# Kernel tuning notes

Measured on AMD Instinct MI355X. Metric: run time of the kernel, lower is better.

Reference implementation:

```python
import jax, jax.numpy as jnp
import numpy as np

B, S, H = 2, 2048, 4096
NH, NKV, HD = 32, 8, 128
THETA = 1000000.0
NEG = jnp.finfo(jnp.float32).min


def setup_inputs() -> dict:
    key = jax.random.key(0)
    ks = jax.random.split(key, 9)
    s = 0.02
    return {
        "hidden_states": jax.random.normal(ks[0], (B, S, H), jnp.float32),
        "position_ids": jnp.tile(jnp.arange(S, dtype=jnp.int32)[None, :], (B, 1)),
        "Wq": jax.random.normal(ks[1], (NH * HD, H), jnp.float32) * s,
        "bq": jax.random.normal(ks[2], (NH * HD,), jnp.float32) * s,
        "Wk": jax.random.normal(ks[3], (NKV * HD, H), jnp.float32) * s,
        "bk": jax.random.normal(ks[4], (NKV * HD,), jnp.float32) * s,
        "Wv": jax.random.normal(ks[5], (NKV * HD, H), jnp.float32) * s,
        "bv": jax.random.normal(ks[6], (NKV * HD,), jnp.float32) * s,
        "Wo": jax.random.normal(ks[7], (H, H), jnp.float32) * s,
        "bo": jax.random.normal(ks[8], (H,), jnp.float32) * s,
    }


def _rotate_half_interleaved(x):
    # y[..., ::2] = -x[..., 1::2]; y[..., 1::2] = x[..., ::2]
    x2 = x.reshape(*x.shape[:-1], -1, 2)
    y = jnp.stack([-x2[..., 1], x2[..., 0]], axis=-1)
    return y.reshape(x.shape)


def reference(hidden_states, position_ids, Wq, bq, Wk, bk, Wv, bv, Wo, bo):
    bsz, q_len, _ = hidden_states.shape
    q = (hidden_states @ Wq.T + bq).reshape(bsz, q_len, NH, HD).transpose(0, 2, 1, 3)
    k = (hidden_states @ Wk.T + bk).reshape(bsz, q_len, NKV, HD).transpose(0, 2, 1, 3)
    v = (hidden_states @ Wv.T + bv).reshape(bsz, q_len, NKV, HD).transpose(0, 2, 1, 3)

    # rotary embedding (interleaved / repeat_interleave variant)
    inv_freq = 1.0 / (THETA ** (jnp.arange(0, HD, 2, dtype=jnp.float32) / HD))
    freqs = position_ids.astype(jnp.float32)[:, :, None] * inv_freq[None, None, :]  # [B,S,HD/2]
    emb = jnp.repeat(freqs, 2, axis=-1)  # [B,S,HD]
    cos = jnp.cos(emb)[:, None, :, :]  # [B,1,S,HD]
    sin = jnp.sin(emb)[:, None, :, :]
    q = q * cos + _rotate_half_interleaved(q) * sin
    k = k * cos + _rotate_half_interleaved(k) * sin

    # GQA: repeat KV heads (repeat_interleave on head axis)
    n_rep = NH // NKV
    k = jnp.repeat(k, n_rep, axis=1)
    v = jnp.repeat(v, n_rep, axis=1)

    scores = jnp.einsum("bhqd,bhkd->bhqk", q, k) / np.sqrt(HD).astype(np.float32)
    causal = jnp.tril(jnp.ones((q_len, q_len), dtype=bool))
    scores = jnp.where(causal[None, None, :, :], scores, NEG)
    attn = jax.nn.softmax(scores.astype(jnp.float32), axis=-1).astype(q.dtype)
    out = jnp.einsum("bhqk,bhkd->bhqd", attn, v)
    out = out.transpose(0, 2, 1, 3).reshape(bsz, q_len, H)
    return out @ Wo.T + bo
```

## Files before the change

### kernel.cpp

```cpp
#include <hip/hip_runtime.h>
#include <stdint.h>

typedef __bf16 bf16x8 __attribute__((ext_vector_type(8)));
typedef float f32x4 __attribute__((ext_vector_type(4)));
typedef float f32x16 __attribute__((ext_vector_type(16)));

#define S_LEN 2048
#define NKVH 8
#define HDIM 128
#define MROWS 4096
#define LDQKV 6144
#define SCALE 0.08838834764831845f
#define C_LOG2 0.1275405707067851f
#define THR_RAW 62.7f

__device__ __forceinline__ unsigned short f2bf(float f) {
  unsigned u = __float_as_uint(f);
  u += 0x7FFFu + ((u >> 16) & 1u);
  return (unsigned short)(u >> 16);
}
__device__ __forceinline__ float bf2f(unsigned short h) {
  return __uint_as_float(((unsigned)h) << 16);
}

__device__ __forceinline__ void gload16(const unsigned short* g, unsigned short* l) {
  __builtin_amdgcn_global_load_lds(
      (__attribute__((address_space(1))) void*)(g),
      (__attribute__((address_space(3))) void*)(l), 16, 0, 0);
}

__global__ void cast_f32_bf16(const float4* __restrict__ in, ushort4* __restrict__ out, int n4) {
  int i = blockIdx.x * 256 + threadIdx.x;
  const int stride = gridDim.x * 256;
  for (; i < n4; i += stride) {
    float4 v = in[i];
    ushort4 o;
    o.x = f2bf(v.x); o.y = f2bf(v.y); o.z = f2bf(v.z); o.w = f2bf(v.w);
    out[i] = o;
  }
}

template <int OUTF>
__global__ __launch_bounds__(512, 2)
void gemm256(const unsigned short* __restrict__ A,
             const unsigned short* __restrict__ Bw,
             const float* __restrict__ bias,
             void* __restrict__ C,
             int M, int N, int K) {
  __shared__ unsigned short lds[2][4][8192];

  const int t = threadIdx.x;
  const int lane = t & 63;
  const int w = t >> 6;
  const int wr = w >> 2, wc = w & 3;
  const int row16 = lane & 15, kgrp = lane >> 4;
  const int m0 = blockIdx.y * 256, n0 = blockIdx.x * 256;

  const int riu = t >> 3;
  const int col = (((t & 7) ^ (riu & 7)) << 3);
  const int rB0 = (riu & 31) + ((riu >> 5) << 6);
  const unsigned short* pA = A + (size_t)(m0 + riu) * K + col;
  const unsigned short* pB = Bw + (size_t)(n0 + rB0) * K + col;

#define STG(nb_, u_, src_)                                                  \
  {                                                                         \
    gload16((src_), &lds[nb_][u_][t * 8]);                                  \
    gload16((src_) + (size_t)128 * K, &lds[nb_][u_][4096 + t * 8]);         \
  }

  const int sw = row16 & 7;
  const int abase = (wr * 64 + row16) * 64;
  const int bbase = (wc * 32 + row16) * 64;

  f32x4 acc[8][4];
#pragma unroll
  for (int i = 0; i < 8; i++)
#pragma unroll
    for (int j = 0; j < 4; j++) acc[i][j] = (f32x4){0.f, 0.f, 0.f, 0.f};

  bf16x8 afr[4][2], bfr[2][2][2];
  const int NT = K >> 6;

  STG(0, 0, pA);
  STG(0, 1, pB);
  STG(0, 2, pB + (size_t)32 * K);
  STG(0, 3, pA + (size_t)64 * K);

  for (int T = 0; T < NT; ++T) {
    const int cb = T & 1, nb = cb ^ 1;
    const unsigned short* Lc = &lds[cb][0][0];
    const size_t kk = (size_t)(T + 1) << 6;
    const bool st = (T + 1 < NT);

    asm volatile("s_waitcnt vmcnt(4)\n\ts_barrier" ::: "memory");
    if (st) STG(nb, 0, pA + kk);
#pragma unroll
    for (int mi = 0; mi < 4; mi++)
#pragma unroll
      for (int ks = 0; ks < 2; ks++)
        afr[mi][ks] = *(const bf16x8*)(Lc + abase + mi * 1024 + ((((ks << 2) + kgrp) ^ sw) << 3));
#pragma unroll
    for (int nj = 0; nj < 2; nj++)
#pragma unroll
      for (int ks = 0; ks < 2; ks++)
        bfr[0][nj][ks] = *(const bf16x8*)(Lc + 8192 + bbase + nj * 1024 + ((((ks << 2) + kgrp) ^ sw) << 3));
    __builtin_amdgcn_s_setprio(1);
#pragma unroll
    for (int mi = 0; mi < 4; mi++)
#pragma unroll
      for (int nj = 0; nj < 2; nj++)
#pragma unroll
        for (int ks = 0; ks < 2; ks++)
          acc[mi][nj] = __builtin_amdgcn_mfma_f32_16x16x32_bf16(afr[mi][ks], bfr[0][nj][ks], acc[mi][nj], 0, 0, 0);
    __builtin_amdgcn_s_setprio(0);

    if (st) {
      asm volatile("s_waitcnt vmcnt(4)\n\ts_barrier" ::: "memory");
      STG(nb, 1, pB + kk);
    } else {
      asm volatile("s_waitcnt vmcnt(2)\n\ts_barrier" ::: "memory");
    }
#pragma unroll
    for (int nj = 0; nj < 2; nj++)
#pragma unroll
      for (int ks = 0; ks < 2; ks++)
        bfr[1][nj][ks] = *(const bf16x8*)(Lc + 16384 + bbase + nj * 1024 + ((((ks << 2) + kgrp) ^ sw) << 3));
    __builtin_amdgcn_s_setprio(1);
#pragma unroll
    for (int mi = 0; mi < 4; mi++)
#pragma unroll
      for (int nj = 0; nj < 2; nj++)
#pragma unroll
        for (int ks = 0; ks < 2; ks++)
          acc[mi][2 + nj] = __builtin_amdgcn_mfma_f32_16x16x32_bf16(afr[mi][ks], bfr[1][nj][ks], acc[mi][2 + nj], 0, 0, 0);
    __builtin_amdgcn_s_setprio(0);

    if (st) {
      asm volatile("s_waitcnt vmcnt(4)\n\ts_barrier" ::: "memory");
      STG(nb, 2, pB + (size_t)32 * K + kk);
    } else {
      asm volatile("s_waitcnt vmcnt(0)\n\ts_barrier" ::: "memory");
    }
#pragma unroll
    for (int mi = 0; mi < 4; mi++)
#pragma unroll
      for (int ks = 0; ks < 2; ks++)
        afr[mi][ks] = *(const bf16x8*)(Lc + 24576 + abase + mi * 1024 + ((((ks << 2) + kgrp) ^ sw) << 3));
    __builtin_amdgcn_s_setprio(1);
#pragma unroll
    for (int mi = 0; mi < 4; mi++)
#pragma unroll
      for (int nj = 0; nj < 2; nj++)
#pragma unroll
        for (int ks = 0; ks < 2; ks++)
          acc[4 + mi][2 + nj] = __builtin_amdgcn_mfma_f32_16x16x32_bf16(afr[mi][ks], bfr[1][nj][ks], acc[4 + mi][2 + nj], 0, 0, 0);
    __builtin_amdgcn_s_setprio(0);

    if (st) {
      asm volatile("s_waitcnt vmcnt(4)\n\ts_barrier" ::: "memory");
      STG(nb, 3, pA + (size_t)64 * K + kk);
    } else {
      asm volatile("s_barrier" ::: "memory");
    }
    __builtin_amdgcn_s_setprio(1);
#pragma unroll
    for (int mi = 0; mi < 4; mi++)
#pragma unroll
      for (int nj = 0; nj < 2; nj++)
#pragma unroll
        for (int ks = 0; ks < 2; ks++)
          acc[4 + mi][nj] = __builtin_amdgcn_mfma_f32_16x16x32_bf16(afr[mi][ks], bfr[0][nj][ks], acc[4 + mi][nj], 0, 0, 0);
    __builtin_amdgcn_s_setprio(0);
  }
#undef STG

#pragma unroll
  for (int MI = 0; MI < 8; MI++) {
#pragma unroll
    for (int NJ = 0; NJ < 4; NJ++) {
      const int gr = m0 + wr * 128 + MI * 16 + kgrp * 4;
      const int gc = n0 + wc * 64 + NJ * 16 + row16;
      const float bv = bias[gc];
#pragma unroll
      for (int jj = 0; jj < 4; jj++) {
        float v = acc[MI][NJ][jj] + bv;
        if (OUTF) ((float*)C)[(size_t)(gr + jj) * N + gc] = v;
        else ((unsigned short*)C)[(size_t)(gr + jj) * N + gc] = f2bf(v);
      }
    }
  }
}

__global__ void rope_kernel(unsigned short* __restrict__ X,
                            const int* __restrict__ pos_ids,
                            int ncols, int ld) {
  const int perrow = ncols >> 3;
  int idx = blockIdx.x * 256 + threadIdx.x;
  const int row = idx / perrow;
  const int c0 = (idx - row * perrow) << 3;
  const float pos = (float)pos_ids[row];
  unsigned short* p = X + (size_t)row * ld + c0;
  uint4 v = *(uint4*)p;
  unsigned short* e = (unsigned short*)&v;
  const int p0 = (c0 & 127) >> 1;
#pragma unroll
  for (int q = 0; q < 4; ++q) {
    const float inv = exp2f(-(float)(p0 + q) * (19.931568569324174f / 64.f));
    const float fr = pos * inv;
    float sn, cs;
    __sincosf(fr, &sn, &cs);
    const float xe = bf2f(e[2 * q]);
    const float xo = bf2f(e[2 * q + 1]);
    e[2 * q]     = f2bf(xe * cs - xo * sn);
    e[2 * q + 1] = f2bf(xo * cs + xe * sn);
  }
  *(uint4*)p = v;
}

__global__ void transpose_v(const unsigned short* __restrict__ V, int ldv,
                            unsigned short* __restrict__ Vt) {
  __shared__ unsigned short tile[32][40];
  const int t = threadIdx.x;
  const int n0 = blockIdx.x * 32;
  const int m0 = blockIdx.y * 32;
  const int r = t >> 3;
  const int c = (t & 7) << 2;
  const unsigned short* src = V + (size_t)(m0 + r) * ldv + n0 + c;
  ushort4 d = *(const ushort4*)src;
  tile[r][c] = d.x; tile[r][c + 1] = d.y; tile[r][c + 2] = d.z; tile[r][c + 3] = d.w;
  __syncthreads();
  const int b = m0 >> 11;
  unsigned short* dst = Vt + (size_t)(b * 1024 + n0 + r) * 2048 + (m0 & 2047) + c;
  ushort4 o;
  o.x = tile[c][r]; o.y = tile[c + 1][r]; o.z = tile[c + 2][r]; o.w = tile[c + 3][r];
  *(ushort4*)dst = o;
}

__global__ __launch_bounds__(512, 2)
void attn_kernel2(const unsigned short* __restrict__ QKV,
                  const unsigned short* __restrict__ Vt,
                  unsigned short* __restrict__ O) {
  __shared__ unsigned short sK[2][64 * 128];
  __shared__ unsigned short sV[2][128 * 64];

  const int t = threadIdx.x;
  const int lane = t & 63;
  const int w = t >> 6;
  const int l31 = lane & 31;
  const int hi = lane >> 5;
  const int qt = 7 - blockIdx.x;
  const int bh = blockIdx.y;
  const int b = bh >> 5, h = bh & 31;
  const int kh = h >> 2;
  const int q0 = qt * 256;
  const int qw = q0 + w * 32;
  const int qg = qw + l31;

  const int ntiles = (q0 + 256) >> 6;
  const int myTiles = (qw + 95) >> 6;

  const int krow0 = t >> 4;
  const int kslot = t & 15;
  const int vrow0 = t >> 3;
  const int vslot = t & 7;
  const unsigned short* Kp = QKV + (size_t)(b * S_LEN) * LDQKV + 4096 + kh * HDIM;
  const unsigned short* Vp = Vt + (size_t)(b * 1024 + kh * HDIM) * 2048;
  const int ksw = (kslot ^ (krow0 & 7)) << 3;
  const int vsw = (vslot ^ (vrow0 & 7)) << 3;
  const unsigned short* KpA = Kp + (size_t)krow0 * LDQKV + ksw;
  const unsigned short* KpB = Kp + (size_t)(krow0 + 32) * LDQKV + ksw;
  const unsigned short* VpA = Vp + (size_t)vrow0 * 2048 + vsw;
  const unsigned short* VpB = Vp + (size_t)(vrow0 + 64) * 2048 + vsw;

#define STAGE(bufi, kv0m)                                              \
  {                                                                    \
    gload16(KpA + (size_t)(kv0m)*LDQKV, &sK[bufi][t * 8]);             \
    gload16(KpB + (size_t)(kv0m)*LDQKV, &sK[bufi][4096 + t * 8]);      \
    gload16(VpA + (kv0m), &sV[bufi][t * 8]);                           \
    gload16(VpB + (kv0m), &sV[bufi][4096 + t * 8]);                    \
  }

  bf16x8 qf[8];
  {
    const unsigned short* qb = QKV + (size_t)(b * S_LEN + qw + l31) * LDQKV + h * HDIM + hi * 8;
#pragma unroll
    for (int kd = 0; kd < 8; kd++) qf[kd] = *(const bf16x8*)(qb + kd * 16);
  }

  f32x16 o[4];
#pragma unroll
  for (int nt = 0; nt < 4; nt++)
#pragma unroll
    for (int r = 0; r < 16; r++) o[nt][r] = 0.f;
  float m = -1e30f, lsum = 0.f;

  const int rw7 = (l31 & 7) << 4;
  const int kswz = (hi << 4) ^ rw7;
  const int kbase0 = l31 * 128;
  const int vbase = l31 * 64;

  STAGE(0, 0);
  int buf = 0;
  for (int it = 0; it < ntiles; ++it) {
    if (it + 1 < ntiles) {
      STAGE(buf ^ 1, (it + 1) << 6);
      asm volatile("s_waitcnt vmcnt(4)" ::: "memory");
    } else {
      asm volatile("s_waitcnt vmcnt(0)" ::: "memory");
    }
    __builtin_amdgcn_s_barrier();

    if (it < myTiles) {
      const unsigned short* sKc = &sK[buf][0];
      const unsigned short* sVc = &sV[buf][0];
      const int kv0 = it << 6;

      f32x16 st[2];
#pragma unroll
      for (int r = 0; r < 16; r++) { st[0][r] = 0.f; st[1][r] = 0.f; }
      __builtin_amdgcn_s_setprio(1);
#pragma unroll
      for (int kd = 0; kd < 8; kd++) {
        bf16x8 k0 = *(const bf16x8*)(sKc + kbase0 + (((kd << 5) ^ kswz) >> 1));
        bf16x8 k1 = *(const bf16x8*)(sKc + 4096 + kbase0 + (((kd << 5) ^ kswz) >> 1));
        st[0] = __builtin_amdgcn_mfma_f32_32x32x16_bf16(k0, qf[kd], st[0], 0, 0, 0);
        st[1] = __builtin_amdgcn_mfma_f32_32x32x16_bf16(k1, qf[kd], st[1], 0, 0, 0);
      }
      __builtin_amdgcn_s_setprio(0);

      if (it == myTiles - 1) {
#pragma unroll
        for (int s2 = 0; s2 < 2; s2++)
#pragma unroll
          for (int r = 0; r < 16; r++) {
            const int kvg = kv0 + s2 * 32 + (r & 3) + 8 * (r >> 2) + 4 * hi;
            if (kvg > qg) st[s2][r] = -1e30f;
          }
      }

      float tmax = st[0][0];
#pragma unroll
      for (int r = 1; r < 16; r++) tmax = fmaxf(tmax, st[0][r]);
#pragma unroll
      for (int r = 0; r < 16; r++) tmax = fmaxf(tmax, st[1][r]);
      tmax = fmaxf(tmax, __shfl_xor(tmax, 32));

      if (!__all(tmax <= m + THR_RAW)) {
        const float mnew = fmaxf(m, tmax);
        const float corr = exp2f((m - mnew) * C_LOG2);
        lsum *= corr;
#pragma unroll
        for (int r = 0; r < 16; r++) {
          const int src = (r & 3) + 8 * (r >> 2) + 4 * hi;
          const float cr = __shfl(corr, src);
#pragma unroll
          for (int nt = 0; nt < 4; nt++) o[nt][r] *= cr;
        }
        m = mnew;
      }
      const float mC = m * C_LOG2;

#pragma unroll
      for (int s2 = 0; s2 < 2; s2++)
#pragma unroll
        for (int r = 0; r < 16; r++) st[s2][r] = exp2f(fmaf(st[s2][r], C_LOG2, -mC));
      float tsum = st[0][0];
#pragma unroll
      for (int r = 1; r < 16; r++) tsum += st[0][r];
#pragma unroll
      for (int r = 0; r < 16; r++) tsum += st[1][r];
      tsum += __shfl_xor(tsum, 32);
      lsum += tsum;

      bf16x8 pa[4];
#pragma unroll
      for (int s2 = 0; s2 < 2; s2++) {
        unsigned pw[8];
#pragma unroll
        for (int i = 0; i < 8; i++)
          asm("v_cvt_pk_bf16_f32 %0, %1, %2" : "=v"(pw[i]) : "v"(st[s2][2 * i]), "v"(st[s2][2 * i + 1]));
        const unsigned x0 = (unsigned)__shfl_xor((int)pw[0], 32);
        const unsigned x1 = (unsigned)__shfl_xor((int)pw[1], 32);
        const unsigned x2 = (unsigned)__shfl_xor((int)pw[2], 32);
        const unsigned x3 = (unsigned)__shfl_xor((int)pw[3], 32);
        const unsigned x4 = (unsigned)__shfl_xor((int)pw[4], 32);
        const unsigned x5 = (unsigned)__shfl_xor((int)pw[5], 32);
        const unsigned x6 = (unsigned)__shfl_xor((int)pw[6], 32);
        const unsigned x7 = (unsigned)__shfl_xor((int)pw[7], 32);
        union { unsigned u[4]; bf16x8 v; } u0, u1;
        u0.u[0] = hi ? x2 : pw[0];
        u0.u[1] = hi ? x3 : pw[1];
        u0.u[2] = hi ? pw[2] : x0;
        u0.u[3] = hi ? pw[3] : x1;
        u1.u[0] = hi ? x6 : pw[4];
        u1.u[1] = hi ? x7 : pw[5];
        u1.u[2] = hi ? pw[6] : x4;
        u1.u[3] = hi ? pw[7] : x5;
        pa[2 * s2] = u0.v; pa[2 * s2 + 1] = u1.v;
      }

      __builtin_amdgcn_s_setprio(1);
#pragma unroll
      for (int nt = 0; nt < 4; nt++) {
        const unsigned short* vr = sVc + vbase + nt * 2048;
#pragma unroll
        for (int ks = 0; ks < 4; ks++) {
          bf16x8 vb = *(const bf16x8*)(vr + (((ks << 5) ^ kswz) >> 1));
          o[nt] = __builtin_amdgcn_mfma_f32_32x32x16_bf16(pa[ks], vb, o[nt], 0, 0, 0);
        }
      }
      __builtin_amdgcn_s_setprio(0);
    }

    asm volatile("" ::: "memory");
    __builtin_amdgcn_s_barrier();
    buf ^= 1;
  }

  const float linv = 1.0f / lsum;
#pragma unroll
  for (int r = 0; r < 16; r++) {
    const int qr = (r & 3) + 8 * (r >> 2) + 4 * hi;
    const float lr = __shfl(linv, qr);
    unsigned short* orow = O + (size_t)(b * S_LEN + qw + qr) * 4096 + h * HDIM + l31;
#pragma unroll
    for (int nt = 0; nt < 4; nt++) orow[nt * 32] = f2bf(o[nt][r] * lr);
  }
#undef STAGE
}

extern "C" void kernel_launch(void* const* d_in, const int* in_sizes, int n_in,
                              void* d_out, int out_size, void* d_ws, size_t ws_size,
                              hipStream_t stream) {
  const float* hs = (const float*)d_in[0];
  const int*  pos = (const int*)d_in[1];
  const float* Wq = (const float*)d_in[2];
  const float* bq = (const float*)d_in[3];
  const float* Wk = (const float*)d_in[4];
  const float* bk = (const float*)d_in[5];
  const float* Wv = (const float*)d_in[6];
  const float* bv = (const float*)d_in[7];
  const float* Wo = (const float*)d_in[8];
  const float* bo = (const float*)d_in[9];
  float* out = (float*)d_out;

  char* ws = (char*)d_ws;
  unsigned short* hbf  = (unsigned short*)(ws);
  unsigned short* Wbuf = (unsigned short*)(ws + 33554432);
  unsigned short* QKV  = (unsigned short*)(ws + 83886080);
  unsigned short* Vtb  = (unsigned short*)(ws + 134217728);
  float*          biasb= (float*)(ws + 142606336);

  cast_f32_bf16<<<2048, 256, 0, stream>>>((const float4*)hs, (ushort4*)hbf, 4194304);
  cast_f32_bf16<<<2048, 256, 0, stream>>>((const float4*)Wq, (ushort4*)Wbuf, 4194304);
  cast_f32_bf16<<<1024, 256, 0, stream>>>((const float4*)Wk, (ushort4*)(Wbuf + 16777216), 1048576);
  cast_f32_bf16<<<1024, 256, 0, stream>>>((const float4*)Wv, (ushort4*)(Wbuf + 20971520), 1048576);
  hipMemcpyAsync(biasb, bq, 4096 * 4, hipMemcpyDeviceToDevice, stream);
  hipMemcpyAsync(biasb + 4096, bk, 1024 * 4, hipMemcpyDeviceToDevice, stream);
  hipMemcpyAsync(biasb + 5120, bv, 1024 * 4, hipMemcpyDeviceToDevice, stream);

  gemm256<0><<<dim3(24, 16), 512, 0, stream>>>(hbf, Wbuf, biasb, QKV, MROWS, LDQKV, 4096);

  cast_f32_bf16<<<2048, 256, 0, stream>>>((const float4*)Wo, (ushort4*)Wbuf, 4194304);

  rope_kernel<<<8192, 256, 0, stream>>>(QKV, pos, 4096, LDQKV);
  rope_kernel<<<2048, 256, 0, stream>>>(QKV + 4096, pos, 1024, LDQKV);

  transpose_v<<<dim3(32, 128), 256, 0, stream>>>(QKV + 5120, LDQKV, Vtb);

  attn_kernel2<<<dim3(8, 64), 512, 0, stream>>>(QKV, Vtb, hbf);

  gemm256<1><<<dim3(16, 16), 512, 0, stream>>>(hbf, Wbuf, bo, out, MROWS, 4096, 4096);
}
```

Measured before the change: 613.9 us.

## Replace double-buffered GEMM LDS staging with a 10-slot ring buffer prefetching deeper

The GEMM's two-buffer, four-unit LDS staging is replaced by a 10-slot circular buffer. Prefetch now runs up to two K-tiles ahead, with waits loosened to vmcnt(8), so more global loads are in flight and MFMA stalls on memory should shrink. LDS use grows from 128KB to 160KB per block, which may limit occupancy under launch_bounds(512,2). The slot rotation and wait counts are delicate and could cause races.

Result: no change. 624.8 us (+1.8%).

```diff
diff --git a/kernel.cpp b/kernel.cpp
--- a/kernel.cpp
+++ b/kernel.cpp
@@ -47,7 +47,7 @@
              const float* __restrict__ bias,
              void* __restrict__ C,
              int M, int N, int K) {
-  __shared__ unsigned short lds[2][4][8192];
+  __shared__ unsigned short lds[10 * 8192];
 
   const int t = threadIdx.x;
   const int lane = t & 63;
@@ -62,10 +62,10 @@
   const unsigned short* pA = A + (size_t)(m0 + riu) * K + col;
   const unsigned short* pB = Bw + (size_t)(n0 + rB0) * K + col;
 
-#define STG(nb_, u_, src_)                                                  \
+#define STGS(sl_, src_)                                                     \
   {                                                                         \
-    gload16((src_), &lds[nb_][u_][t * 8]);                                  \
-    gload16((src_) + (size_t)128 * K, &lds[nb_][u_][4096 + t * 8]);         \
+    gload16((src_), &lds[(sl_) * 8192 + t * 8]);                            \
+    gload16((src_) + (size_t)128 * K, &lds[(sl_) * 8192 + 4096 + t * 8]);   \
   }
 
   const int sw = row16 & 7;
@@ -81,29 +81,44 @@
   bf16x8 afr[4][2], bfr[2][2][2];
   const int NT = K >> 6;
 
-  STG(0, 0, pA);
-  STG(0, 1, pB);
-  STG(0, 2, pB + (size_t)32 * K);
-  STG(0, 3, pA + (size_t)64 * K);
-
+  STGS(0, pA);
+  STGS(1, pB);
+  STGS(2, pB + (size_t)32 * K);
+  STGS(3, pA + (size_t)64 * K);
+  STGS(4, pA + 64);
+  STGS(5, pB + 64);
+
+  int rb = 0;
   for (int T = 0; T < NT; ++T) {
-    const int cb = T & 1, nb = cb ^ 1;
-    const unsigned short* Lc = &lds[cb][0][0];
-    const size_t kk = (size_t)(T + 1) << 6;
-    const bool st = (T + 1 < NT);
-
-    asm volatile("s_waitcnt vmcnt(4)\n\ts_barrier" ::: "memory");
-    if (st) STG(nb, 0, pA + kk);
+    int s1 = rb + 1; if (s1 >= 10) s1 -= 10;
+    int s2 = rb + 2; if (s2 >= 10) s2 -= 10;
+    int s3 = rb + 3; if (s3 >= 10) s3 -= 10;
+    int s6 = rb + 6; if (s6 >= 10) s6 -= 10;
+    int s7 = rb + 7; if (s7 >= 10) s7 -= 10;
+    int s8 = rb + 8; if (s8 >= 10) s8 -= 10;
+    int s9 = rb + 9; if (s9 >= 10) s9 -= 10;
+    const bool st1 = (T < NT - 1);
+    const bool st2 = (T < NT - 2);
+    const size_t k1 = (size_t)(T + 1) << 6;
+    const size_t k2 = (size_t)(T + 2) << 6;
+    const unsigned short* U0 = &lds[rb * 8192];
+    const unsigned short* U1 = &lds[s1 * 8192];
+    const unsigned short* U2 = &lds[s2 * 8192];
+    const unsigned short* U3 = &lds[s3 * 8192];
+
+    if (st1) { asm volatile("s_waitcnt vmcnt(8)\n\ts_barrier" ::: "memory"); }
+    else     { asm volatile("s_waitcnt vmcnt(4)\n\ts_barrier" ::: "memory"); }
+    if (st1) STGS(s6, pB + (size_t)32 * K + k1);
 #pragma unroll
     for (int mi = 0; mi < 4; mi++)
 #pragma unroll
       for (int ks = 0; ks < 2; ks++)
-        afr[mi][ks] = *(const bf16x8*)(Lc + abase + mi * 1024 + ((((ks << 2) + kgrp) ^ sw) << 3));
+        afr[mi][ks] = *(const bf16x8*)(U0 + abase + mi * 1024 + ((((ks << 2) + kgrp) ^ sw) << 3));
 #pragma unroll
     for (int nj = 0; nj < 2; nj++)
 #pragma unroll
       for (int ks = 0; ks < 2; ks++)
-        bfr[0][nj][ks] = *(const bf16x8*)(Lc + 8192 + bbase + nj * 1024 + ((((ks << 2) + kgrp) ^ sw) << 3));
+        bfr[0][nj][ks] = *(const bf16x8*)(U1 + bbase + nj * 1024 + ((((ks << 2) + kgrp) ^ sw) << 3));
     __builtin_amdgcn_s_setprio(1);
 #pragma unroll
     for (int mi = 0; mi < 4; mi++)
@@ -114,17 +129,14 @@
           acc[mi][nj] = __builtin_amdgcn_mfma_f32_16x16x32_bf16(afr[mi][ks], bfr[0][nj][ks], acc[mi][nj], 0, 0, 0);
     __builtin_amdgcn_s_setprio(0);
 
-    if (st) {
-      asm volatile("s_waitcnt vmcnt(4)\n\ts_barrier" ::: "memory");
-      STG(nb, 1, pB + kk);
-    } else {
-      asm volatile("s_waitcnt vmcnt(2)\n\ts_barrier" ::: "memory");
-    }
+    if (st1) { asm volatile("s_waitcnt vmcnt(8)\n\ts_barrier" ::: "memory"); }
+    else     { asm volatile("s_waitcnt vmcnt(2)\n\ts_barrier" ::: "memory"); }
+    if (st1) STGS(s7, pA + (size_t)64 * K + k1);
 #pragma unroll
     for (int nj = 0; nj < 2; nj++)
 #pragma unroll
       for (int ks = 0; ks < 2; ks++)
-        bfr[1][nj][ks] = *(const bf16x8*)(Lc + 16384 + bbase + nj * 1024 + ((((ks << 2) + kgrp) ^ sw) << 3));
+        bfr[1][nj][ks] = *(const bf16x8*)(U2 + bbase + nj * 1024 + ((((ks << 2) + kgrp) ^ sw) << 3));
     __builtin_amdgcn_s_setprio(1);
 #pragma unroll
     for (int mi = 0; mi < 4; mi++)
@@ -135,17 +147,14 @@
           acc[mi][2 + nj] = __builtin_amdgcn_mfma_f32_16x16x32_bf16(afr[mi][ks], bfr[1][nj][ks], acc[mi][2 + nj], 0, 0, 0);
     __builtin_amdgcn_s_setprio(0);
 
-    if (st) {
-      asm volatile("s_waitcnt vmcnt(4)\n\ts_barrier" ::: "memory");
-      STG(nb, 2, pB + (size_t)32 * K + kk);
-    } else {
-      asm volatile("s_waitcnt vmcnt(0)\n\ts_barrier" ::: "memory");
-    }
+    if (st1) { asm volatile("s_waitcnt vmcnt(8)\n\ts_barrier" ::: "memory"); }
+    else     { asm volatile("s_waitcnt vmcnt(0)\n\ts_barrier" ::: "memory"); }
+    if (st2) STGS(s8, pA + k2);
 #pragma unroll
     for (int mi = 0; mi < 4; mi++)
 #pragma unroll
       for (int ks = 0; ks < 2; ks++)
-        afr[mi][ks] = *(const bf16x8*)(Lc + 24576 + abase + mi * 1024 + ((((ks << 2) + kgrp) ^ sw) << 3));
+        afr[mi][ks] = *(const bf16x8*)(U3 + abase + mi * 1024 + ((((ks << 2) + kgrp) ^ sw) << 3));
     __builtin_amdgcn_s_setprio(1);
 #pragma unroll
     for (int mi = 0; mi < 4; mi++)
@@ -156,12 +165,7 @@
           acc[4 + mi][2 + nj] = __builtin_amdgcn_mfma_f32_16x16x32_bf16(afr[mi][ks], bfr[1][nj][ks], acc[4 + mi][2 + nj], 0, 0, 0);
     __builtin_amdgcn_s_setprio(0);
 
-    if (st) {
-      asm volatile("s_waitcnt vmcnt(4)\n\ts_barrier" ::: "memory");
-      STG(nb, 3, pA + (size_t)64 * K + kk);
-    } else {
-      asm volatile("s_barrier" ::: "memory");
-    }
+    if (st2) STGS(s9, pB + k2);
     __builtin_amdgcn_s_setprio(1);
 #pragma unroll
     for (int mi = 0; mi < 4; mi++)
@@ -171,8 +175,10 @@
         for (int ks = 0; ks < 2; ks++)
           acc[4 + mi][nj] = __builtin_amdgcn_mfma_f32_16x16x32_bf16(afr[mi][ks], bfr[0][nj][ks], acc[4 + mi][nj], 0, 0, 0);
     __builtin_amdgcn_s_setprio(0);
-  }
-#undef STG
+
+    rb += 4; if (rb >= 10) rb -= 10;
+  }
+#undef STGS
 
 #pragma unroll
   for (int MI = 0; MI < 8; MI++) {
```

## Split QKV projection into Q GEMM and separate 128-row-tile KV GEMM

Applied to the files above, without the earlier changes.

The fused QKV GEMM previously ran 24x16=384 tiles of 256x256, which is a poor fit for the GPU's compute-unit count (1.5 waves). Now Q uses 256 tiles of 256x256, and K/V use a new gemm128 kernel with 128x256 tiles (256 blocks) and triple-buffered LDS. This aims to fix the wave-quantization tail. The cost is an extra launch, a second kernel design to maintain, and lower arithmetic intensity per tile in the KV part.

Result: faster. 587.0 us (-4.4%).

```diff
diff --git a/kernel.cpp b/kernel.cpp
--- a/kernel.cpp
+++ b/kernel.cpp
@@ -46,7 +46,7 @@
              const unsigned short* __restrict__ Bw,
              const float* __restrict__ bias,
              void* __restrict__ C,
-             int M, int N, int K) {
+             int ldc, int K) {
   __shared__ unsigned short lds[2][4][8192];
 
   const int t = threadIdx.x;
@@ -184,8 +184,106 @@
 #pragma unroll
       for (int jj = 0; jj < 4; jj++) {
         float v = acc[MI][NJ][jj] + bv;
-        if (OUTF) ((float*)C)[(size_t)(gr + jj) * N + gc] = v;
-        else ((unsigned short*)C)[(size_t)(gr + jj) * N + gc] = f2bf(v);
+        if (OUTF) ((float*)C)[(size_t)(gr + jj) * ldc + gc] = v;
+        else ((unsigned short*)C)[(size_t)(gr + jj) * ldc + gc] = f2bf(v);
+      }
+    }
+  }
+}
+
+template <int OUTF>
+__global__ __launch_bounds__(512, 2)
+void gemm128(const unsigned short* __restrict__ A,
+             const unsigned short* __restrict__ Bw,
+             const float* __restrict__ bias,
+             void* __restrict__ C,
+             int ldc, int K) {
+  __shared__ unsigned short lds[3 * 24576];
+
+  const int t = threadIdx.x;
+  const int lane = t & 63;
+  const int w = t >> 6;
+  const int wr = w >> 2, wc = w & 3;
+  const int row16 = lane & 15, kgrp = lane >> 4;
+  const int m0 = blockIdx.y * 128, n0 = blockIdx.x * 256;
+
+  const int riu = t >> 3;
+  const int col = (((t & 7) ^ (riu & 7)) << 3);
+  const unsigned short* pA = A + (size_t)(m0 + riu) * K + col;
+  const unsigned short* pB = Bw + (size_t)(n0 + riu) * K + col;
+
+#define STG6(bo_, kk_)                                                      \
+  {                                                                         \
+    gload16(pA + (kk_), &lds[(bo_) + t * 8]);                               \
+    gload16(pA + (size_t)64 * K + (kk_), &lds[(bo_) + 4096 + t * 8]);       \
+    gload16(pB + (kk_), &lds[(bo_) + 8192 + t * 8]);                        \
+    gload16(pB + (size_t)64 * K + (kk_), &lds[(bo_) + 12288 + t * 8]);      \
+    gload16(pB + (size_t)128 * K + (kk_), &lds[(bo_) + 16384 + t * 8]);     \
+    gload16(pB + (size_t)192 * K + (kk_), &lds[(bo_) + 20480 + t * 8]);     \
+  }
+
+  const int sw = row16 & 7;
+  const int abase = (wr * 64 + row16) * 64;
+  const int bbase = 8192 + (wc * 64 + row16) * 64;
+
+  f32x4 acc[4][4];
+#pragma unroll
+  for (int i = 0; i < 4; i++)
+#pragma unroll
+    for (int j = 0; j < 4; j++) acc[i][j] = (f32x4){0.f, 0.f, 0.f, 0.f};
+
+  bf16x8 afr[4][2], bfr[4][2];
+  const int NT = K >> 6;
+
+  STG6(0, 0);
+  STG6(24576, 64);
+
+  int rbc = 0;
+  int rbs = 2;
+  for (int T = 0; T < NT; ++T) {
+    if (T < NT - 1) { asm volatile("s_waitcnt vmcnt(6)\n\ts_barrier" ::: "memory"); }
+    else            { asm volatile("s_waitcnt vmcnt(0)\n\ts_barrier" ::: "memory"); }
+    if (T + 2 < NT) STG6(rbs * 24576, (size_t)(T + 2) << 6);
+    const unsigned short* Lc = &lds[rbc * 24576];
+
+#pragma unroll
+    for (int mi = 0; mi < 4; mi++)
+#pragma unroll
+      for (int ks = 0; ks < 2; ks++)
+        afr[mi][ks] = *(const bf16x8*)(Lc + abase + mi * 1024 + ((((ks << 2) + kgrp) ^ sw) << 3));
+#pragma unroll
+    for (int nj = 0; nj < 4; nj++)
+#pragma unroll
+      for (int ks = 0; ks < 2; ks++)
+        bfr[nj][ks] = *(const bf16x8*)(Lc + bbase + nj * 1024 + ((((ks << 2) + kgrp) ^ sw) << 3));
+
+    __builtin_amdgcn_s_setprio(1);
+#pragma unroll
+    for (int mi = 0; mi < 4; mi++)
+#pragma unroll
+      for (int nj = 0; nj < 4; nj++)
+#pragma unroll
+        for (int ks = 0; ks < 2; ks++)
+          acc[mi][nj] = __builtin_amdgcn_mfma_f32_16x16x32_bf16(afr[mi][ks], bfr[nj][ks], acc[mi][nj], 0, 0, 0);
+    __builtin_amdgcn_s_setprio(0);
+
+    rbc++; if (rbc == 3) rbc = 0;
+    rbs++; if (rbs == 3) rbs = 0;
+  }
+#undef STG6
+
+#pragma unroll
+  for (int MI = 0; MI < 4; MI++) {
+#pragma unroll
+    for (int NJ = 0; NJ < 4; NJ++) {
+      const int gr = m0 + wr * 64 + MI * 16 + kgrp * 4;
+      const int gc = n0 + wc * 64 + NJ * 16 + row16;
+      const float bv = bias[gc];
+#pragma unroll
+      for (int jj = 0; jj < 4; jj++) {
+        float v = acc[MI][NJ][jj] + bv;
+        if (OUTF) ((float*)C)[(size_t)(gr + jj) * ldc + gc] = v;
+        else ((unsigned short*)C)[(size_t)(gr + jj) * ldc + gc] = f2bf(v);
       }
     }
   }
@@ -459,7 +557,8 @@
   hipMemcpyAsync(biasb + 4096, bk, 1024 * 4, hipMemcpyDeviceToDevice, stream);
   hipMemcpyAsync(biasb + 5120, bv, 1024 * 4, hipMemcpyDeviceToDevice, stream);
 
-  gemm256<0><<<dim3(24, 16), 512, 0, stream>>>(hbf, Wbuf, biasb, QKV, MROWS, LDQKV, 4096);
+  gemm256<0><<<dim3(16, 16), 512, 0, stream>>>(hbf, Wbuf, biasb, QKV, LDQKV, 4096);
+  gemm128<0><<<dim3(8, 32), 512, 0, stream>>>(hbf, Wbuf + 16777216, biasb + 4096, QKV + 4096, LDQKV, 4096);
 
   cast_f32_bf16<<<2048, 256, 0, stream>>>((const float4*)Wo, (ushort4*)Wbuf, 4194304);
 
@@ -470,5 +569,5 @@
 
   attn_kernel2<<<dim3(8, 64), 512, 0, stream>>>(QKV, Vtb, hbf);
 
-  gemm256<1><<<dim3(16, 16), 512, 0, stream>>>(hbf, Wbuf, bo, out, MROWS, 4096, 4096);
-}
+  gemm256<1><<<dim3(16, 16), 512, 0, stream>>>(hbf, Wbuf, bo, out, 4096, 4096);
+}
```
